# Optimization experiments

Hardware: AMD Instinct MI355X
Metric: run time of the kernel (lower is better)

## Reference

```python
import jax, jax.numpy as jnp
import numpy as np

D_MODEL, D_STATE, EXPAND = 768, 16, 2
D_INNER = D_MODEL * EXPAND
B, L = 2, 2048


def setup_inputs() -> dict:
    key = jax.random.key(0)
    ks = jax.random.split(key, 10)
    s = 0.02  # init scale for projection weights
    return {
        "x": jax.random.normal(ks[0], (B, L, D_MODEL), jnp.float32),
        "in_w": jax.random.normal(ks[1], (D_MODEL, 2 * D_INNER), jnp.float32) * s,
        "conv_w": jax.random.normal(ks[2], (D_INNER, 1, 3), jnp.float32) * 0.1,
        "conv_b": jnp.zeros((D_INNER,), jnp.float32),
        "xproj_w": jax.random.normal(ks[3], (D_INNER, 2 * D_STATE), jnp.float32) * s,
        "dt_w": jax.random.normal(ks[4], (D_INNER, D_INNER), jnp.float32) * s,
        "dt_b": jnp.zeros((D_INNER,), jnp.float32),
        "A_log": jax.random.normal(ks[5], (D_INNER, D_STATE), jnp.float32) * 0.01,
        "D": jnp.ones((D_INNER,), jnp.float32),
        "out_w": jax.random.normal(ks[6], (D_INNER, D_MODEL), jnp.float32) * s,
    }


def reference(x, in_w, conv_w, conv_b, xproj_w, dt_w, dt_b, A_log, D, out_w):
    d_inner = conv_w.shape[0]
    d_state = A_log.shape[1]

    xz = x @ in_w                                   # [B,L,2*d_inner]
    x_c, z = jnp.split(xz, 2, axis=-1)

    # depthwise conv1d, kernel 3, padding 1
    xc = jnp.transpose(x_c, (0, 2, 1))              # [B,d_inner,L]
    xc = jax.lax.conv_general_dilated(
        xc, conv_w, window_strides=(1,), padding=[(1, 1)],
        feature_group_count=d_inner,
        dimension_numbers=("NCH", "OIH", "NCH"))
    xc = xc + conv_b[None, :, None]
    xc = jax.nn.silu(jnp.transpose(xc, (0, 2, 1)))  # [B,L,d_inner]

    Bs, Cs = jnp.split(xc @ xproj_w, 2, axis=-1)    # each [B,L,d_state]
    delta = jax.nn.softplus(xc @ dt_w + dt_b)       # [B,L,d_inner]
    A = -jnp.exp(A_log.astype(jnp.float32))         # [d_inner,d_state]

    deltaA = jnp.exp(jnp.einsum("bld,dn->bldn", delta, A))      # [B,L,d_inner,d_state]
    deltaBx = jnp.einsum("bld,bln->bldn", delta * xc, Bs)        # [B,L,d_inner,d_state]

    def step(h, inp):
        dA_t, dBx_t, c_t = inp                      # [B,d,n],[B,d,n],[B,n]
        h = dA_t * h + dBx_t
        y_t = jnp.einsum("bdn,bn->bd", h, c_t)
        return h, y_t

    h0 = jnp.zeros((x.shape[0], d_inner, d_state), xc.dtype)
    xs = (jnp.moveaxis(deltaA, 1, 0), jnp.moveaxis(deltaBx, 1, 0), jnp.moveaxis(Cs, 1, 0))
    _, ys = jax.lax.scan(step, h0, xs)              # ys: [L,B,d_inner]
    y = jnp.moveaxis(ys, 0, 1) + D * xc             # skip connection

    y = y * jax.nn.silu(z)
    return y @ out_w                                # [B,L,d_model]
```

## Files before the change

### kernel.cpp

```cpp
#include <hip/hip_runtime.h>
#include <cmath>

#define DMODEL 768
#define DINNER 1536
#define NSTATE 16
#define SEQL   2048
#define NCHUNK 32
#define CHLEN  64

#define DT_F32  0
#define DT_BF16 1
#define DT_ZERO 2

typedef __bf16 bf16x8 __attribute__((ext_vector_type(8)));
typedef float  f32x4  __attribute__((ext_vector_type(4)));

typedef __attribute__((address_space(3))) unsigned short lds_us;
typedef const __attribute__((address_space(1))) unsigned short glob_us;

__device__ __forceinline__ void async_cp16(glob_us* g, lds_us* l) {
    __builtin_amdgcn_global_load_lds((const __attribute__((address_space(1))) void*)g,
                                     (__attribute__((address_space(3))) void*)l, 16, 0, 0);
}

__device__ __forceinline__ float bf2f(unsigned short h) {
    union { unsigned u; float f; } v; v.u = ((unsigned)h) << 16; return v.f;
}
__device__ __forceinline__ unsigned short f2bf(float f) {
    union { float f; unsigned u; } v; v.f = f;
    unsigned r = (v.u + 0x7FFFu + ((v.u >> 16) & 1u)) >> 16;
    return (unsigned short)r;
}
__device__ int detect_dtype(const void* p) {
    const unsigned* u = (const unsigned*)p;
    int nzlo = 0, band = 0, anynz = 0;
    for (int i = 0; i < 64; ++i) {
        unsigned w = u[i];
        anynz |= (w != 0);
        unsigned lo = w & 0xFFFFu;
        if (lo) {
            ++nzlo;
            unsigned e8 = (lo >> 7) & 0xFF;
            if (e8 >= 0x60 && e8 <= 0x8E) ++band;
        }
    }
    if (nzlo >= 8) return (band * 2 > nzlo) ? DT_BF16 : DT_F32;
    return anynz ? DT_F32 : DT_ZERO;
}
__device__ __forceinline__ float LD(const void* p, size_t i, int dt) {
    if (dt == DT_BF16) return bf2f(((const unsigned short*)p)[i]);
    if (dt == DT_F32)  return ((const float*)p)[i];
    return 0.f;
}

__global__ __launch_bounds__(256) void prep_kernel(
    const void* __restrict__ x, const void* __restrict__ in_w,
    const void* __restrict__ cw, const void* __restrict__ cb,
    const void* __restrict__ xp, const void* __restrict__ dt_w,
    const void* __restrict__ db, const void* __restrict__ Al,
    const void* __restrict__ Dv, const void* __restrict__ out_w,
    unsigned short* __restrict__ xb, unsigned short* __restrict__ inT,
    unsigned short* __restrict__ dtT, unsigned short* __restrict__ outT,
    float* __restrict__ pf)
{
    __shared__ unsigned short tile[32][33];
    __shared__ int dts[6];
    const int blk = blockIdx.x;
    const int t   = threadIdx.x;

    if (blk < 324) {
        if (t == 0) {
            dts[0] = detect_dtype(cw); dts[1] = detect_dtype(cb);
            dts[2] = detect_dtype(db); dts[3] = detect_dtype(Al);
            dts[4] = detect_dtype(Dv); dts[5] = detect_dtype(xp);
        }
        __syncthreads();
        int g = blk * 256 + t;
        if (g >= 82944) return;
        const void* src; int local; int which;
        if      (g <  4608) { src = cw; local = g;         which = 0; }
        else if (g <  6144) { src = cb; local = g - 4608;  which = 1; }
        else if (g <  7680) { src = db; local = g - 6144;  which = 2; }
        else if (g < 32256) { src = Al; local = g - 7680;  which = 3; }
        else if (g < 33792) { src = Dv; local = g - 32256; which = 4; }
        else                { src = xp; local = g - 33792; which = 5; }
        pf[g] = LD(src, local, dts[which]);
    } else if (blk < 3396) {
        if (t == 0) dts[0] = detect_dtype(x);
        __syncthreads();
        const int dt = dts[0];
        size_t i = ((size_t)(blk - 324) * 256 + t) * 4;
        ushort4 o;
        o.x = f2bf(LD(x, i + 0, dt)); o.y = f2bf(LD(x, i + 1, dt));
        o.z = f2bf(LD(x, i + 2, dt)); o.w = f2bf(LD(x, i + 3, dt));
        *(ushort4*)&xb[i] = o;
    } else {
        const void* src; unsigned short* dst; int R, C, tx_n, idx;
        if (blk < 5700)      { src = in_w;  dst = inT;  R = 768;  C = 3072; tx_n = 96; idx = blk - 3396; }
        else if (blk < 8004) { src = dt_w;  dst = dtT;  R = 1536; C = 1536; tx_n = 48; idx = blk - 5700; }
        else                 { src = out_w; dst = outT; R = 1536; C = 768;  tx_n = 24; idx = blk - 8004; }
        if (t == 0) dts[0] = detect_dtype(src);
        __syncthreads();
        const int dt = dts[0];
        const int tx = t & 31, ty = t >> 5;
        const int bx = (idx % tx_n) * 32, by = (idx / tx_n) * 32;
        #pragma unroll
        for (int i = 0; i < 4; ++i) {
            int r = by + ty + i * 8;
            tile[ty + i * 8][tx] = f2bf(LD(src, (size_t)r * C + bx + tx, dt));
        }
        __syncthreads();
        #pragma unroll
        for (int i = 0; i < 4; ++i) {
            int c = bx + ty + i * 8;
            dst[(size_t)c * R + by + tx] = tile[tx][ty + i * 8];
        }
    }
}

template<int EPI>
__global__ __launch_bounds__(256) void gemm_kernel(
    const unsigned short* __restrict__ A, const unsigned short* __restrict__ Bt,
    void* __restrict__ C0, void* __restrict__ C1, const float* __restrict__ biasf,
    int M, int N, int K)
{
    __shared__ __align__(16) unsigned short As[2][2][128 * 32];
    __shared__ __align__(16) unsigned short Bs[2][2][64 * 32];
    const int t    = threadIdx.x;
    const int m0   = blockIdx.x * 128;
    const int n0   = blockIdx.y * 64;
    const int w    = t >> 6;
    const int lane = t & 63;
    const int wm   = (w >> 1) * 64, wn = (w & 1) * 32;
    const int lm   = lane & 15, quad = lane >> 4;
    const int srow = lane >> 2;
    const int sg   = lane & 3;

    f32x4 acc[4][2] = {};

    auto stage = [&](int k0, int q) {
        #pragma unroll
        for (int ph = 0; ph < 2; ++ph) {
            #pragma unroll
            for (int h = 0; h < 2; ++h) {
                int row = w * 32 + h * 16 + srow;
                int kg  = (sg - (row >> 1)) & 3;
                async_cp16((glob_us*)&A[(size_t)(m0 + row) * K + k0 + ph * 32 + kg * 8],
                           (lds_us*)&As[q][ph][(w * 32 + h * 16) * 32]);
            }
            int brow = w * 16 + srow;
            int bkg  = (sg - (brow >> 1)) & 3;
            async_cp16((glob_us*)&Bt[(size_t)(n0 + brow) * K + k0 + ph * 32 + bkg * 8],
                       (lds_us*)&Bs[q][ph][(w * 16) * 32]);
        }
    };

    stage(0, 0);

    int p = 0;
    for (int k0 = 0; k0 < K; k0 += 64) {
        __syncthreads();
        if (k0 + 64 < K) stage(k0 + 64, p ^ 1);
        #pragma unroll
        for (int ph = 0; ph < 2; ++ph) {
            bf16x8 af[4], bfr[2];
            #pragma unroll
            for (int i = 0; i < 4; ++i) {
                int row = wm + i * 16 + lm;
                int g   = (quad + (row >> 1)) & 3;
                af[i] = *(const bf16x8*)&As[p][ph][row * 32 + g * 8];
            }
            #pragma unroll
            for (int j = 0; j < 2; ++j) {
                int row = wn + j * 16 + lm;
                int g   = (quad + (row >> 1)) & 3;
                bfr[j] = *(const bf16x8*)&Bs[p][ph][row * 32 + g * 8];
            }
            #pragma unroll
            for (int i = 0; i < 4; ++i)
                #pragma unroll
                for (int j = 0; j < 2; ++j)
                    acc[i][j] = __builtin_amdgcn_mfma_f32_16x16x32_bf16(af[i], bfr[j], acc[i][j], 0, 0, 0);
        }
        p ^= 1;
    }

    const int half = N >> 1;
    #pragma unroll
    for (int i = 0; i < 4; ++i) {
        #pragma unroll
        for (int j = 0; j < 2; ++j) {
            int col = n0 + wn + j * 16 + lm;
            #pragma unroll
            for (int r = 0; r < 4; ++r) {
                int row = m0 + wm + i * 16 + quad * 4 + r;
                float v = acc[i][j][r];
                if (EPI == 1) {
                    v += biasf[col];
                    float sp = (v > 20.f) ? v : log1pf(__expf(v));
                    ((unsigned short*)C0)[(size_t)row * N + col] = f2bf(sp);
                } else if (EPI == 2) {
                    ((float*)C0)[(size_t)row * N + col] = v;
                } else {
                    if (col < half) {
                        ((unsigned short*)C0)[(size_t)row * half + col] = f2bf(v);
                    } else {
                        float s = v / (1.f + __expf(-v));
                        ((unsigned short*)C1)[(size_t)row * half + col - half] = f2bf(s);
                    }
                }
            }
        }
    }
}

__global__ __launch_bounds__(256) void conv_silu_kernel(
    const unsigned short* __restrict__ xcpre, const float* __restrict__ cwf,
    const float* __restrict__ cbf, unsigned short* __restrict__ xcb)
{
    int idx = blockIdx.x * 256 + threadIdx.x;
    int d   = idx % DINNER;
    int row = idx / DINNER;
    int l   = row % SEQL;
    size_t base = (size_t)row * DINNER + d;
    float acc = cbf[d];
    if (l > 0)        acc += bf2f(xcpre[base - DINNER]) * cwf[d * 3 + 0];
    acc += bf2f(xcpre[base]) * cwf[d * 3 + 1];
    if (l < SEQL - 1) acc += bf2f(xcpre[base + DINNER]) * cwf[d * 3 + 2];
    float s = acc / (1.f + __expf(-acc));
    xcb[base] = f2bf(s);
}

__global__ __launch_bounds__(128) void xproj_kernel(
    const unsigned short* __restrict__ xcb, const float* __restrict__ wf,
    float* __restrict__ BC)
{
    __shared__ float red[4][32][4];
    const int t = threadIdx.x;
    const int s = t & 31, part = t >> 5;
    const int row0 = blockIdx.x * 4;
    float acc[4] = {0.f, 0.f, 0.f, 0.f};
    for (int k = part * 384; k < (part + 1) * 384; ++k) {
        float wv = wf[k * 32 + s];
        #pragma unroll
        for (int r = 0; r < 4; ++r)
            acc[r] += bf2f(xcb[(size_t)(row0 + r) * DINNER + k]) * wv;
    }
    #pragma unroll
    for (int r = 0; r < 4; ++r) red[part][s][r] = acc[r];
    __syncthreads();
    if (t < 32) {
        #pragma unroll
        for (int r = 0; r < 4; ++r)
            BC[(size_t)(row0 + r) * 32 + t] =
                red[0][t][r] + red[1][t][r] + red[2][t][r] + red[3][t][r];
    }
}

struct GrpA { unsigned short dv[4], xv[4]; f32x4 Bv[4]; };
struct GrpC { unsigned short dv[4], xv[4], zv[4]; f32x4 Bv[4], Cv[4]; };

__device__ __forceinline__ void ldA(GrpA& gp, const unsigned short* pd,
    const unsigned short* px, const float* pbc, int l) {
    #pragma unroll
    for (int j = 0; j < 4; ++j) {
        size_t o = (size_t)(l + j) * DINNER;
        gp.dv[j] = pd[o];
        gp.xv[j] = px[o];
        gp.Bv[j] = *(const f32x4*)&pbc[(size_t)(l + j) * 32];
    }
}
__device__ __forceinline__ void ldC(GrpC& gp, const unsigned short* pd,
    const unsigned short* px, const unsigned short* pz, const float* pbc, int l) {
    #pragma unroll
    for (int j = 0; j < 4; ++j) {
        size_t o = (size_t)(l + j) * DINNER;
        gp.dv[j] = pd[o];
        gp.xv[j] = px[o];
        gp.zv[j] = pz[o];
        gp.Bv[j] = *(const f32x4*)&pbc[(size_t)(l + j) * 32];
        gp.Cv[j] = *(const f32x4*)&pbc[(size_t)(l + j) * 32 + 16];
    }
}
__device__ __forceinline__ void stepA(const GrpA& gp, const f32x4 A1,
    f32x4& h, float& sdv) {
    #pragma unroll
    for (int j = 0; j < 4; ++j) {
        float dv = bf2f(gp.dv[j]);
        float xv = bf2f(gp.xv[j]);
        float dx = dv * xv;
        sdv += dv;
        f32x4 e;
        e[0] = __expf(dv * A1[0]); e[1] = __expf(dv * A1[1]);
        e[2] = __expf(dv * A1[2]); e[3] = __expf(dv * A1[3]);
        h = e * h + dx * gp.Bv[j];
    }
}
__device__ __forceinline__ void stepC(const GrpC& gp, const f32x4 A1,
    f32x4& h, float Dd, int q, unsigned short* py, int l) {
    #pragma unroll
    for (int j = 0; j < 4; ++j) {
        float dv = bf2f(gp.dv[j]);
        float xv = bf2f(gp.xv[j]);
        float dx = dv * xv;
        f32x4 e;
        e[0] = __expf(dv * A1[0]); e[1] = __expf(dv * A1[1]);
        e[2] = __expf(dv * A1[2]); e[3] = __expf(dv * A1[3]);
        h = e * h + dx * gp.Bv[j];
        f32x4 yv = h * gp.Cv[j];
        float y = yv[0] + yv[1] + yv[2] + yv[3];
        y += __shfl_xor(y, 1);
        y += __shfl_xor(y, 2);
        if (q == 0) {
            float zv = bf2f(gp.zv[j]);
            py[(size_t)(l + j) * DINNER] = f2bf((y + Dd * xv) * zv);
        }
    }
}

__global__ __launch_bounds__(256) void scan_phase_a(
    const unsigned short* __restrict__ dlt, const unsigned short* __restrict__ xcb,
    const float* __restrict__ BC, const float* __restrict__ A_log_f,
    unsigned short* __restrict__ P, float* __restrict__ S)
{
    int g = blockIdx.x * 256 + threadIdx.x;
    int q = g & 3;
    int d = (g >> 2) % DINNER;
    int c = ((g >> 2) / DINNER) % NCHUNK;
    int b = (g >> 2) / (DINNER * NCHUNK);
    f32x4 al = *(const f32x4*)&A_log_f[d * 16 + q * 4];
    f32x4 A1;
    A1[0] = -__expf(al[0]); A1[1] = -__expf(al[1]);
    A1[2] = -__expf(al[2]); A1[3] = -__expf(al[3]);
    f32x4 h = (f32x4){0.f, 0.f, 0.f, 0.f};
    float sdv = 0.f;
    const int row0 = b * SEQL + c * CHLEN;
    const unsigned short* pd = dlt + (size_t)row0 * DINNER + d;
    const unsigned short* px = xcb + (size_t)row0 * DINNER + d;
    const float* pbc = BC + (size_t)row0 * 32 + q * 4;

    GrpA ga, gb;
    ldA(ga, pd, px, pbc, 0);
    for (int l0 = 0; l0 < CHLEN; l0 += 8) {
        ldA(gb, pd, px, pbc, l0 + 4);
        stepA(ga, A1, h, sdv);
        if (l0 + 8 < CHLEN) ldA(ga, pd, px, pbc, l0 + 8);
        stepA(gb, A1, h, sdv);
    }

    size_t idx = (((size_t)(b * NCHUNK + c)) * DINNER + d) * 16 + q * 4;
    *(f32x4*)&S[idx] = h;
    ushort4 pq;
    pq.x = f2bf(__expf(sdv * A1[0]));
    pq.y = f2bf(__expf(sdv * A1[1]));
    pq.z = f2bf(__expf(sdv * A1[2]));
    pq.w = f2bf(__expf(sdv * A1[3]));
    *(ushort4*)&P[idx] = pq;
}

__global__ __launch_bounds__(256) void scan_combine(
    const unsigned short* __restrict__ P, float* __restrict__ S)
{
    int t = blockIdx.x * 256 + threadIdx.x;
    int b = t / (DINNER * NSTATE);
    int dn = t % (DINNER * NSTATE);
    const size_t stride = (size_t)(DINNER * NSTATE);
    size_t idx = (size_t)b * NCHUNK * stride + dn;
    float Pv = bf2f(P[idx]);
    float Sv = S[idx];
    float H = 0.f;
    for (int c = 0; c < NCHUNK; ++c) {
        float Pn = 0.f, Sn = 0.f;
        if (c + 1 < NCHUNK) {
            Pn = bf2f(P[idx + stride]);
            Sn = S[idx + stride];
        }
        S[idx] = H;
        H = Pv * H + Sv;
        Pv = Pn; Sv = Sn;
        idx += stride;
    }
}

__global__ __launch_bounds__(256) void scan_phase_c(
    const unsigned short* __restrict__ dlt, const unsigned short* __restrict__ xcb,
    const float* __restrict__ BC, const unsigned short* __restrict__ zg,
    const float* __restrict__ A_log_f, const float* __restrict__ D_f,
    const float* __restrict__ Hin, unsigned short* __restrict__ yg)
{
    int g = blockIdx.x * 256 + threadIdx.x;
    int q = g & 3;
    int d = (g >> 2) % DINNER;
    int c = ((g >> 2) / DINNER) % NCHUNK;
    int b = (g >> 2) / (DINNER * NCHUNK);
    f32x4 al = *(const f32x4*)&A_log_f[d * 16 + q * 4];
    f32x4 A1;
    A1[0] = -__expf(al[0]); A1[1] = -__expf(al[1]);
    A1[2] = -__expf(al[2]); A1[3] = -__expf(al[3]);
    size_t hidx = (((size_t)(b * NCHUNK + c)) * DINNER + d) * 16 + q * 4;
    f32x4 h = *(const f32x4*)&Hin[hidx];
    const float Dd = D_f[d];
    const int row0 = b * SEQL + c * CHLEN;
    const unsigned short* pd = dlt + (size_t)row0 * DINNER + d;
    const unsigned short* px = xcb + (size_t)row0 * DINNER + d;
    const unsigned short* pz = zg  + (size_t)row0 * DINNER + d;
    unsigned short* py = yg + (size_t)row0 * DINNER + d;
    const float* pbc = BC + (size_t)row0 * 32 + q * 4;

    GrpC ga, gb;
    ldC(ga, pd, px, pz, pbc, 0);
    for (int l0 = 0; l0 < CHLEN; l0 += 8) {
        ldC(gb, pd, px, pz, pbc, l0 + 4);
        stepC(ga, A1, h, Dd, q, py, l0);
        if (l0 + 8 < CHLEN) ldC(ga, pd, px, pz, pbc, l0 + 8);
        stepC(gb, A1, h, Dd, q, py, l0 + 4);
    }
}

__global__ void guard_kernel(float* out, int code)
{
    if (threadIdx.x == 0 && blockIdx.x == 0 && code) out[0] = (float)code;
}

extern "C" void kernel_launch(void* const* d_in, const int* in_sizes, int n_in,
                              void* d_out, int out_size, void* d_ws, size_t ws_size,
                              hipStream_t stream) {
    static const int EXPECTED[10] = {3145728, 2359296, 4608, 1536, 49152,
                                     2359296, 1536, 24576, 1536, 1179648};
    bool ok = (n_in == 10);
    if (ok) for (int i = 0; i < 10; ++i) ok = ok && (in_sizes[i] == EXPECTED[i]);
    int code = 0;
    if (!ok) code = 2000;
    else if (ws_size < 67895296ULL) code = 3000;
    if (code) { guard_kernel<<<1, 64, 0, stream>>>((float*)d_out, code); return; }

    const void* x       = d_in[0];
    const void* in_w    = d_in[1];
    const void* conv_w  = d_in[2];
    const void* conv_b  = d_in[3];
    const void* xproj_w = d_in[4];
    const void* dt_w    = d_in[5];
    const void* dt_b    = d_in[6];
    const void* A_log   = d_in[7];
    const void* Dvec    = d_in[8];
    const void* out_w   = d_in[9];

    char* ws = (char*)d_ws;
    float* conv_w_f = (float*)(ws + 0);
    float* conv_b_f = (float*)(ws + 18432);
    float* dt_b_f   = (float*)(ws + 24576);
    float* A_log_f  = (float*)(ws + 30720);
    float* D_f      = (float*)(ws + 129024);
    float* xproj_f  = (float*)(ws + 135168);
    unsigned short* xb    = (unsigned short*)(ws + 524288);
    unsigned short* inT   = (unsigned short*)(ws + 6815744);
    unsigned short* yg    = (unsigned short*)(ws + 524288);
    unsigned short* dtT   = (unsigned short*)(ws + 13107200);
    unsigned short* outT  = (unsigned short*)(ws + 17825792);
    unsigned short* xcpre = (unsigned short*)(ws + 20185088);
    unsigned short* dlt   = xcpre;
    float*          BC    = (float*)(ws + 32768000);
    unsigned short* zg    = (unsigned short*)(ws + 33292288);
    unsigned short* xcb   = (unsigned short*)(ws + 45875200);
    float*          scanS = (float*)(ws + 58458112);
    unsigned short* scanP = (unsigned short*)(ws + 64749568);

    prep_kernel<<<9156, 256, 0, stream>>>(x, in_w, conv_w, conv_b, xproj_w, dt_w,
                                          dt_b, A_log, Dvec, out_w,
                                          xb, inT, dtT, outT, (float*)ws);

    gemm_kernel<3><<<dim3(32, 48), 256, 0, stream>>>(xb, inT, (void*)xcpre, (void*)zg,
                                                     nullptr, 4096, 3072, 768);
    conv_silu_kernel<<<(4096 * DINNER) / 256, 256, 0, stream>>>(xcpre, conv_w_f, conv_b_f, xcb);
    xproj_kernel<<<1024, 128, 0, stream>>>(xcb, xproj_f, BC);
    gemm_kernel<1><<<dim3(32, 24), 256, 0, stream>>>(xcb, dtT, (void*)dlt, nullptr,
                                                     dt_b_f, 4096, 1536, 1536);
    scan_phase_a<<<1536, 256, 0, stream>>>(dlt, xcb, BC, A_log_f, scanP, scanS);
    scan_combine<<<192, 256, 0, stream>>>(scanP, scanS);
    scan_phase_c<<<1536, 256, 0, stream>>>(dlt, xcb, BC, zg, A_log_f, D_f, scanS, yg);
    gemm_kernel<2><<<dim3(32, 12), 256, 0, stream>>>(yg, outT, d_out, nullptr,
                                                    nullptr, 4096, 768, 1536);
}
```

Measured before the change: 337.3 us.

## Vectorize prep conversions, precompute exp2-scaled A, spread phase-C output writes across lanes

The prep kernel now converts x with 8 elements per thread using float4 loads, and transposes weights in 64x64 tiles with vector loads and stores. This cuts the block count and the scalar memory traffic. A is precomputed as -exp(A_log)*log2(e) once in prep, so the scan kernels use the hardware exp2 directly instead of recomputing exp(A_log) and calling __expf. In scan phase C, each of the four lanes in a group now loads one z value and writes one output row, instead of only lane q==0 loading all z and writing everything. This balances the stores but adds a select per step.

```diff
diff --git a/kernel.cpp b/kernel.cpp
--- a/kernel.cpp
+++ b/kernel.cpp
@@ -63,7 +63,7 @@
     unsigned short* __restrict__ dtT, unsigned short* __restrict__ outT,
     float* __restrict__ pf)
 {
-    __shared__ unsigned short tile[32][33];
+    __shared__ unsigned short tile[64][68];
     __shared__ int dts[6];
     const int blk = blockIdx.x;
     const int t   = threadIdx.x;
@@ -84,36 +84,62 @@
         else if (g < 32256) { src = Al; local = g - 7680;  which = 3; }
         else if (g < 33792) { src = Dv; local = g - 32256; which = 4; }
         else                { src = xp; local = g - 33792; which = 5; }
-        pf[g] = LD(src, local, dts[which]);
-    } else if (blk < 3396) {
+        float v = LD(src, local, dts[which]);
+        if (which == 3) v = -__expf(v) * 1.44269504f;
+        pf[g] = v;
+    } else if (blk < 1860) {
         if (t == 0) dts[0] = detect_dtype(x);
         __syncthreads();
         const int dt = dts[0];
-        size_t i = ((size_t)(blk - 324) * 256 + t) * 4;
-        ushort4 o;
-        o.x = f2bf(LD(x, i + 0, dt)); o.y = f2bf(LD(x, i + 1, dt));
-        o.z = f2bf(LD(x, i + 2, dt)); o.w = f2bf(LD(x, i + 3, dt));
-        *(ushort4*)&xb[i] = o;
+        size_t i = ((size_t)(blk - 324) * 256 + t) * 8;
+        ushort4 o0, o1;
+        if (dt == DT_F32) {
+            float4 a = *(const float4*)((const float*)x + i);
+            float4 b = *(const float4*)((const float*)x + i + 4);
+            o0.x = f2bf(a.x); o0.y = f2bf(a.y); o0.z = f2bf(a.z); o0.w = f2bf(a.w);
+            o1.x = f2bf(b.x); o1.y = f2bf(b.y); o1.z = f2bf(b.z); o1.w = f2bf(b.w);
+        } else if (dt == DT_BF16) {
+            o0 = *(const ushort4*)((const unsigned short*)x + i);
+            o1 = *(const ushort4*)((const unsigned short*)x + i + 4);
+        } else {
+            o0 = (ushort4){0,0,0,0}; o1 = (ushort4){0,0,0,0};
+        }
+        *(ushort4*)&xb[i] = o0;
+        *(ushort4*)&xb[i + 4] = o1;
     } else {
         const void* src; unsigned short* dst; int R, C, tx_n, idx;
-        if (blk < 5700)      { src = in_w;  dst = inT;  R = 768;  C = 3072; tx_n = 96; idx = blk - 3396; }
-        else if (blk < 8004) { src = dt_w;  dst = dtT;  R = 1536; C = 1536; tx_n = 48; idx = blk - 5700; }
-        else                 { src = out_w; dst = outT; R = 1536; C = 768;  tx_n = 24; idx = blk - 8004; }
+        if (blk < 2436)      { src = in_w;  dst = inT;  R = 768;  C = 3072; tx_n = 48; idx = blk - 1860; }
+        else if (blk < 3012) { src = dt_w;  dst = dtT;  R = 1536; C = 1536; tx_n = 24; idx = blk - 2436; }
+        else                 { src = out_w; dst = outT; R = 1536; C = 768;  tx_n = 12; idx = blk - 3012; }
         if (t == 0) dts[0] = detect_dtype(src);
         __syncthreads();
         const int dt = dts[0];
-        const int tx = t & 31, ty = t >> 5;
-        const int bx = (idx % tx_n) * 32, by = (idx / tx_n) * 32;
+        const int tx = t & 15, ty = t >> 4;
+        const int bx = (idx % tx_n) * 64, by = (idx / tx_n) * 64;
         #pragma unroll
         for (int i = 0; i < 4; ++i) {
-            int r = by + ty + i * 8;
-            tile[ty + i * 8][tx] = f2bf(LD(src, (size_t)r * C + bx + tx, dt));
+            int rl = ty + i * 16;
+            size_t soff = (size_t)(by + rl) * C + bx + tx * 4;
+            ushort4 hv;
+            if (dt == DT_F32) {
+                float4 v = *(const float4*)((const float*)src + soff);
+                hv.x = f2bf(v.x); hv.y = f2bf(v.y); hv.z = f2bf(v.z); hv.w = f2bf(v.w);
+            } else if (dt == DT_BF16) {
+                hv = *(const ushort4*)((const unsigned short*)src + soff);
+            } else {
+                hv = (ushort4){0,0,0,0};
+            }
+            *(ushort4*)&tile[rl][tx * 4] = hv;
         }
         __syncthreads();
         #pragma unroll
         for (int i = 0; i < 4; ++i) {
-            int c = bx + ty + i * 8;
-            dst[(size_t)c * R + by + tx] = tile[tx][ty + i * 8];
+            int cl = ty + i * 16;
+            int m0 = tx * 4;
+            ushort4 o;
+            o.x = tile[m0 + 0][cl]; o.y = tile[m0 + 1][cl];
+            o.z = tile[m0 + 2][cl]; o.w = tile[m0 + 3][cl];
+            *(ushort4*)&dst[(size_t)(bx + cl) * R + by + m0] = o;
         }
     }
 }
@@ -258,7 +284,7 @@
 }
 
 struct GrpA { unsigned short dv[4], xv[4]; f32x4 Bv[4]; };
-struct GrpC { unsigned short dv[4], xv[4], zv[4]; f32x4 Bv[4], Cv[4]; };
+struct GrpC { unsigned short dv[4], xv[4], zq; f32x4 Bv[4], Cv[4]; };
 
 __device__ __forceinline__ void ldA(GrpA& gp, const unsigned short* pd,
     const unsigned short* px, const float* pbc, int l) {
@@ -271,18 +297,19 @@
     }
 }
 __device__ __forceinline__ void ldC(GrpC& gp, const unsigned short* pd,
-    const unsigned short* px, const unsigned short* pz, const float* pbc, int l) {
+    const unsigned short* px, const unsigned short* pz, const float* pbc,
+    int l, int q) {
     #pragma unroll
     for (int j = 0; j < 4; ++j) {
         size_t o = (size_t)(l + j) * DINNER;
         gp.dv[j] = pd[o];
         gp.xv[j] = px[o];
-        gp.zv[j] = pz[o];
         gp.Bv[j] = *(const f32x4*)&pbc[(size_t)(l + j) * 32];
         gp.Cv[j] = *(const f32x4*)&pbc[(size_t)(l + j) * 32 + 16];
     }
-}
-__device__ __forceinline__ void stepA(const GrpA& gp, const f32x4 A1,
+    gp.zq = pz[(size_t)(l + q) * DINNER];
+}
+__device__ __forceinline__ void stepA(const GrpA& gp, const f32x4 A2,
     f32x4& h, float& sdv) {
     #pragma unroll
     for (int j = 0; j < 4; ++j) {
@@ -291,31 +318,35 @@
         float dx = dv * xv;
         sdv += dv;
         f32x4 e;
-        e[0] = __expf(dv * A1[0]); e[1] = __expf(dv * A1[1]);
-        e[2] = __expf(dv * A1[2]); e[3] = __expf(dv * A1[3]);
+        e[0] = __builtin_amdgcn_exp2f(dv * A2[0]);
+        e[1] = __builtin_amdgcn_exp2f(dv * A2[1]);
+        e[2] = __builtin_amdgcn_exp2f(dv * A2[2]);
+        e[3] = __builtin_amdgcn_exp2f(dv * A2[3]);
         h = e * h + dx * gp.Bv[j];
     }
 }
-__device__ __forceinline__ void stepC(const GrpC& gp, const f32x4 A1,
+__device__ __forceinline__ void stepC(const GrpC& gp, const f32x4 A2,
     f32x4& h, float Dd, int q, unsigned short* py, int l) {
+    float yq = 0.f, xq = 0.f;
     #pragma unroll
     for (int j = 0; j < 4; ++j) {
         float dv = bf2f(gp.dv[j]);
         float xv = bf2f(gp.xv[j]);
         float dx = dv * xv;
         f32x4 e;
-        e[0] = __expf(dv * A1[0]); e[1] = __expf(dv * A1[1]);
-        e[2] = __expf(dv * A1[2]); e[3] = __expf(dv * A1[3]);
+        e[0] = __builtin_amdgcn_exp2f(dv * A2[0]);
+        e[1] = __builtin_amdgcn_exp2f(dv * A2[1]);
+        e[2] = __builtin_amdgcn_exp2f(dv * A2[2]);
+        e[3] = __builtin_amdgcn_exp2f(dv * A2[3]);
         h = e * h + dx * gp.Bv[j];
         f32x4 yv = h * gp.Cv[j];
         float y = yv[0] + yv[1] + yv[2] + yv[3];
         y += __shfl_xor(y, 1);
         y += __shfl_xor(y, 2);
-        if (q == 0) {
-            float zv = bf2f(gp.zv[j]);
-            py[(size_t)(l + j) * DINNER] = f2bf((y + Dd * xv) * zv);
-        }
-    }
+        if (j == q) { yq = y; xq = xv; }
+    }
+    float zv = bf2f(gp.zq);
+    py[(size_t)(l + q) * DINNER] = f2bf((yq + Dd * xq) * zv);
 }
 
 __global__ __launch_bounds__(256) void scan_phase_a(
@@ -328,10 +359,7 @@
     int d = (g >> 2) % DINNER;
     int c = ((g >> 2) / DINNER) % NCHUNK;
     int b = (g >> 2) / (DINNER * NCHUNK);
-    f32x4 al = *(const f32x4*)&A_log_f[d * 16 + q * 4];
-    f32x4 A1;
-    A1[0] = -__expf(al[0]); A1[1] = -__expf(al[1]);
-    A1[2] = -__expf(al[2]); A1[3] = -__expf(al[3]);
+    f32x4 A2 = *(const f32x4*)&A_log_f[d * 16 + q * 4];
     f32x4 h = (f32x4){0.f, 0.f, 0.f, 0.f};
     float sdv = 0.f;
     const int row0 = b * SEQL + c * CHLEN;
@@ -343,18 +371,18 @@
     ldA(ga, pd, px, pbc, 0);
     for (int l0 = 0; l0 < CHLEN; l0 += 8) {
         ldA(gb, pd, px, pbc, l0 + 4);
-        stepA(ga, A1, h, sdv);
+        stepA(ga, A2, h, sdv);
         if (l0 + 8 < CHLEN) ldA(ga, pd, px, pbc, l0 + 8);
-        stepA(gb, A1, h, sdv);
+        stepA(gb, A2, h, sdv);
     }
 
     size_t idx = (((size_t)(b * NCHUNK + c)) * DINNER + d) * 16 + q * 4;
     *(f32x4*)&S[idx] = h;
     ushort4 pq;
-    pq.x = f2bf(__expf(sdv * A1[0]));
-    pq.y = f2bf(__expf(sdv * A1[1]));
-    pq.z = f2bf(__expf(sdv * A1[2]));
-    pq.w = f2bf(__expf(sdv * A1[3]));
+    pq.x = f2bf(__builtin_amdgcn_exp2f(sdv * A2[0]));
+    pq.y = f2bf(__builtin_amdgcn_exp2f(sdv * A2[1]));
+    pq.z = f2bf(__builtin_amdgcn_exp2f(sdv * A2[2]));
+    pq.w = f2bf(__builtin_amdgcn_exp2f(sdv * A2[3]));
     *(ushort4*)&P[idx] = pq;
 }
 
@@ -393,10 +421,7 @@
     int d = (g >> 2) % DINNER;
     int c = ((g >> 2) / DINNER) % NCHUNK;
     int b = (g >> 2) / (DINNER * NCHUNK);
-    f32x4 al = *(const f32x4*)&A_log_f[d * 16 + q * 4];
-    f32x4 A1;
-    A1[0] = -__expf(al[0]); A1[1] = -__expf(al[1]);
-    A1[2] = -__expf(al[2]); A1[3] = -__expf(al[3]);
+    f32x4 A2 = *(const f32x4*)&A_log_f[d * 16 + q * 4];
     size_t hidx = (((size_t)(b * NCHUNK + c)) * DINNER + d) * 16 + q * 4;
     f32x4 h = *(const f32x4*)&Hin[hidx];
     const float Dd = D_f[d];
@@ -408,12 +433,12 @@
     const float* pbc = BC + (size_t)row0 * 32 + q * 4;
 
     GrpC ga, gb;
-    ldC(ga, pd, px, pz, pbc, 0);
+    ldC(ga, pd, px, pz, pbc, 0, q);
     for (int l0 = 0; l0 < CHLEN; l0 += 8) {
-        ldC(gb, pd, px, pz, pbc, l0 + 4);
-        stepC(ga, A1, h, Dd, q, py, l0);
-        if (l0 + 8 < CHLEN) ldC(ga, pd, px, pz, pbc, l0 + 8);
-        stepC(gb, A1, h, Dd, q, py, l0 + 4);
+        ldC(gb, pd, px, pz, pbc, l0 + 4, q);
+        stepC(ga, A2, h, Dd, q, py, l0);
+        if (l0 + 8 < CHLEN) ldC(ga, pd, px, pz, pbc, l0 + 8, q);
+        stepC(gb, A2, h, Dd, q, py, l0 + 4);
     }
 }
 
@@ -465,7 +490,7 @@
     float*          scanS = (float*)(ws + 58458112);
     unsigned short* scanP = (unsigned short*)(ws + 64749568);
 
-    prep_kernel<<<9156, 256, 0, stream>>>(x, in_w, conv_w, conv_b, xproj_w, dt_w,
+    prep_kernel<<<3300, 256, 0, stream>>>(x, in_w, conv_w, conv_b, xproj_w, dt_w,
                                           dt_b, A_log, Dvec, out_w,
                                           xb, inT, dtT, outT, (float*)ws);
 
```

Result: faster. 322.5 us (-4.4%).
